# Optimization experiments

Hardware: AMD Instinct MI355X
Metric: run time of the kernel (lower is better)

## Reference

```python
import jax, jax.numpy as jnp
import numpy as np

D_MODEL = 1024
N_HEADS = 16
HEAD_DIM = D_MODEL // N_HEADS


def setup_inputs() -> dict:
    key = jax.random.key(0)
    ks = jax.random.split(key, 9)
    s = 1.0 / np.sqrt(D_MODEL)
    inp = {
        "x": jax.random.normal(ks[0], (4, 2048, D_MODEL), dtype=jnp.float32),
        "wq": jax.random.uniform(ks[1], (D_MODEL, D_MODEL), jnp.float32, -s, s),
        "bq": jax.random.uniform(ks[2], (D_MODEL,), jnp.float32, -s, s),
        "wk": jax.random.uniform(ks[3], (D_MODEL, D_MODEL), jnp.float32, -s, s),
        "bk": jax.random.uniform(ks[4], (D_MODEL,), jnp.float32, -s, s),
        "wv": jax.random.uniform(ks[5], (D_MODEL, D_MODEL), jnp.float32, -s, s),
        "bv": jax.random.uniform(ks[6], (D_MODEL,), jnp.float32, -s, s),
        "wo": jax.random.uniform(ks[7], (D_MODEL, D_MODEL), jnp.float32, -s, s),
        "bo": jax.random.uniform(ks[8], (D_MODEL,), jnp.float32, -s, s),
    }
    return inp


def reference(x, wq, bq, wk, bk, wv, bv, wo, bo):
    b, s, d = x.shape
    h, hd = N_HEADS, HEAD_DIM
    # projections (torch Linear: y = x @ W.T + b; here weights stored as [in, out])
    q = (x @ wq + bq).reshape(b, s, h, hd).transpose(0, 2, 1, 3)  # [b,h,s,hd]
    k = (x @ wk + bk).reshape(b, s, h, hd).transpose(0, 2, 1, 3)
    v = (x @ wv + bv).reshape(b, s, h, hd).transpose(0, 2, 1, 3)
    scores = jnp.einsum("bhqd,bhkd->bhqk", q, k) / jnp.sqrt(jnp.float32(hd))
    causal = jnp.tril(jnp.ones((s, s), dtype=bool))
    scores = jnp.where(causal, scores, -jnp.inf)
    weights = jax.nn.softmax(scores, axis=-1)
    attn = jnp.einsum("bhqk,bhkd->bhqd", weights, v)  # [b,h,s,hd]
    attn = attn.transpose(0, 2, 1, 3).reshape(b, s, d)
    return attn @ wo + bo
```

## Files before the change

### kernel.cpp

```cpp
#include <hip/hip_runtime.h>
#include <cstddef>

#define D_MODEL 1024
#define NH 16
#define HD 64
#define BATCH 4
#define SEQ 2048
#define MTOT (BATCH * SEQ)

typedef _Float16 half8 __attribute__((ext_vector_type(8)));
typedef _Float16 half4v __attribute__((ext_vector_type(4)));
typedef float f32x4 __attribute__((ext_vector_type(4)));

#if __has_builtin(__builtin_amdgcn_exp2f)
#define EXP2(x) __builtin_amdgcn_exp2f(x)
#else
#define EXP2(x) __expf((x)*0.69314718056f)
#endif

__global__ __launch_bounds__(256) void prep(
    const float* __restrict__ x, _Float16* __restrict__ xh,
    const float* __restrict__ W0, const float* __restrict__ W1,
    const float* __restrict__ W2, const float* __restrict__ W3,
    _Float16* __restrict__ T0, _Float16* __restrict__ T1,
    _Float16* __restrict__ T2, _Float16* __restrict__ T3)
{
    __shared__ float T[64][65];
    const int bid = blockIdx.x;
    if (bid < 256) {
        const size_t base = (size_t)bid * 4096 + threadIdx.x;
#pragma unroll
        for (int it = 0; it < 16; ++it) {
            const size_t i = base + (size_t)it * 256;
            const float4* p = (const float4*)x + 2 * i;
            float4 a = p[0], b = p[1];
            half8 h;
            h[0] = (_Float16)a.x; h[1] = (_Float16)a.y; h[2] = (_Float16)a.z; h[3] = (_Float16)a.w;
            h[4] = (_Float16)b.x; h[5] = (_Float16)b.y; h[6] = (_Float16)b.z; h[7] = (_Float16)b.w;
            *((half8*)xh + i) = h;
        }
    } else {
        const int t = bid - 256;
        const int mtx = t >> 8;
        const float* W = (mtx == 0) ? W0 : (mtx == 1) ? W1 : (mtx == 2) ? W2 : W3;
        _Float16*   Wt = (mtx == 0) ? T0 : (mtx == 1) ? T1 : (mtx == 2) ? T2 : T3;
        const int tile = t & 255;
        const int k0 = (tile >> 4) * 64, n0 = (tile & 15) * 64;
        const int r = threadIdx.x >> 4, c4 = (threadIdx.x & 15) * 4;

#pragma unroll
        for (int i = 0; i < 4; ++i) {
            float4 v = *(const float4*)(W + (size_t)(k0 + r + 16 * i) * 1024 + n0 + c4);
            T[r + 16 * i][c4 + 0] = v.x; T[r + 16 * i][c4 + 1] = v.y;
            T[r + 16 * i][c4 + 2] = v.z; T[r + 16 * i][c4 + 3] = v.w;
        }
        __syncthreads();
#pragma unroll
        for (int i = 0; i < 4; ++i) {
            const int n = r + 16 * i;
            half4v h;
            h[0] = (_Float16)T[c4 + 0][n]; h[1] = (_Float16)T[c4 + 1][n];
            h[2] = (_Float16)T[c4 + 2][n]; h[3] = (_Float16)T[c4 + 3][n];
            *(half4v*)(Wt + (size_t)(n0 + n) * 1024 + k0 + c4) = h;
        }
    }
}

template <int QKV>
__global__ __launch_bounds__(256) void gemm_mfma(
    const _Float16* __restrict__ A,
    const _Float16* __restrict__ Bt0, const _Float16* __restrict__ Bt1, const _Float16* __restrict__ Bt2,
    const float* __restrict__ bi0, const float* __restrict__ bi1, const float* __restrict__ bi2,
    void* __restrict__ C0, void* __restrict__ C1, void* __restrict__ C2)
{
    const int L = blockIdx.x;
    const int y = L & 63;
    const int c_ = L >> 6;
    const int z  = QKV ? (c_ >> 3) : 0;
    const int xb = QKV ? (c_ & 7) : c_;

    const _Float16* Bt = (z == 0) ? Bt0 : (z == 1) ? Bt1 : Bt2;
    const float*   bia = (z == 0) ? bi0 : (z == 1) ? bi1 : bi2;
    void*            C = (z == 0) ? C0  : (z == 1) ? C1  : C2;

    __shared__ _Float16 As[128][72];
    __shared__ _Float16 Bs[128][72];

    const int tid  = threadIdx.x;
    const int w    = tid >> 6;
    const int lane = tid & 63;
    const int l15  = lane & 15;
    const int lg   = lane >> 4;
    const int m0 = y * 128;
    const int n0 = xb * 128;
    const int wm = (w >> 1) * 64, wn = (w & 1) * 64;

    const int srow = tid >> 3;
    const int scol = (tid & 7) * 8;

    const _Float16* Ab = A + (size_t)(m0 + srow) * 1024 + scol;
    const _Float16* Bb = Bt + (size_t)(n0 + srow) * 1024 + scol;

    half8 aR[4], bR[4];
#pragma unroll
    for (int i = 0; i < 4; ++i) {
        aR[i] = *(const half8*)(Ab + (size_t)(32 * i) * 1024);
        bR[i] = *(const half8*)(Bb + (size_t)(32 * i) * 1024);
    }

    f32x4 acc[4][4];
#pragma unroll
    for (int i = 0; i < 4; ++i)
#pragma unroll
        for (int j = 0; j < 4; ++j) { acc[i][j][0] = 0.f; acc[i][j][1] = 0.f; acc[i][j][2] = 0.f; acc[i][j][3] = 0.f; }

    for (int kt = 0; kt < 16; ++kt) {
        __syncthreads();
#pragma unroll
        for (int i = 0; i < 4; ++i) {
            *(half8*)&As[srow + 32 * i][scol] = aR[i];
            *(half8*)&Bs[srow + 32 * i][scol] = bR[i];
        }
        __syncthreads();
        if (kt < 15) {
            const int k0 = (kt + 1) * 64;
#pragma unroll
            for (int i = 0; i < 4; ++i) {
                aR[i] = *(const half8*)(Ab + (size_t)(32 * i) * 1024 + k0);
                bR[i] = *(const half8*)(Bb + (size_t)(32 * i) * 1024 + k0);
            }
        }
#pragma unroll
        for (int c = 0; c < 2; ++c) {
            half8 af[4], bf[4];
#pragma unroll
            for (int i = 0; i < 4; ++i) af[i] = *(const half8*)&As[wm + 16 * i + l15][32 * c + 8 * lg];
#pragma unroll
            for (int j = 0; j < 4; ++j) bf[j] = *(const half8*)&Bs[wn + 16 * j + l15][32 * c + 8 * lg];
#pragma unroll
            for (int i = 0; i < 4; ++i)
#pragma unroll
                for (int j = 0; j < 4; ++j)
                    acc[i][j] = __builtin_amdgcn_mfma_f32_16x16x32_f16(af[i], bf[j], acc[i][j], 0, 0, 0);
        }
    }

    float bv[4];
#pragma unroll
    for (int j = 0; j < 4; ++j) bv[j] = bia[n0 + wn + 16 * j + l15];

#pragma unroll
    for (int i = 0; i < 4; ++i)
#pragma unroll
        for (int j = 0; j < 4; ++j)
#pragma unroll
            for (int r = 0; r < 4; ++r) {
                const int m = m0 + wm + 16 * i + 4 * lg + r;
                const int n = n0 + wn + 16 * j + l15;
                const float val = acc[i][j][r] + bv[j];
                if (QKV) {
                    const int bb = m >> 11, ss = m & 2047, hh = n >> 6, hd = n & 63;
                    if (z < 2)
                        ((_Float16*)C)[((size_t)(bb * NH + hh) * SEQ + ss) * HD + hd] = (_Float16)val;
                    else
                        ((_Float16*)C)[((size_t)(bb * NH + hh) * HD + hd) * SEQ + ss] = (_Float16)val;
                } else {
                    ((float*)C)[(size_t)m * 1024 + n] = val;
                }
            }
}

__global__ __launch_bounds__(256, 4) void attn_fwd_mfma(
    const _Float16* __restrict__ Q, const _Float16* __restrict__ K,
    const _Float16* __restrict__ Vt, _Float16* __restrict__ O)
{
    __shared__ _Float16 Ks[64][80];
    __shared__ _Float16 Vs[64][80];
    __shared__ _Float16 Ps[4][16][80];

    const int tid  = threadIdx.x;
    const int w    = tid >> 6;
    const int lane = tid & 63;
    const int l15  = lane & 15;
    const int lg   = lane >> 4;

    const int bh = blockIdx.y;
    const int b  = bh >> 4, h = bh & 15;

    const _Float16* Qb  = Q  + (size_t)bh * SEQ * HD;
    const _Float16* Kb  = K  + (size_t)bh * SEQ * HD;
    const _Float16* Vtb = Vt + (size_t)bh * HD * SEQ;

    const int srow = tid >> 3;
    const int scol = (tid & 7) * 8;

    for (int pass = 0; pass < 2; ++pass) {
        const int qt = pass ? (int)blockIdx.x : (31 - (int)blockIdx.x);
        const int q0 = qt * 64;
        const int ntiles = qt + 1;

        half8 qa[2];
        {
            const _Float16* qp = Qb + (size_t)(q0 + 16 * w + l15) * HD + 8 * lg;
            qa[0] = *(const half8*)(qp);
            qa[1] = *(const half8*)(qp + 32);
#pragma unroll
            for (int c = 0; c < 2; ++c)
#pragma unroll
                for (int j = 0; j < 8; ++j)
                    qa[c][j] = (_Float16)((float)qa[c][j] * 0.18033688f);
        }

        f32x4 o_[4];
#pragma unroll
        for (int ft = 0; ft < 4; ++ft) { o_[ft][0] = 0.f; o_[ft][1] = 0.f; o_[ft][2] = 0.f; o_[ft][3] = 0.f; }
        float lp[4] = {0.f, 0.f, 0.f, 0.f};

        half8 kreg[2], vreg[2];
#pragma unroll
        for (int j = 0; j < 2; ++j) {
            kreg[j] = *(const half8*)(Kb  + (size_t)(srow + 32 * j) * HD + scol);
            vreg[j] = *(const half8*)(Vtb + (size_t)(srow + 32 * j) * SEQ + scol);
        }

        for (int kt = 0; kt < ntiles; ++kt) {
            __syncthreads();
#pragma unroll
            for (int j = 0; j < 2; ++j) {
                *(half8*)&Ks[srow + 32 * j][scol] = kreg[j];
                *(half8*)&Vs[srow + 32 * j][scol] = vreg[j];
            }
            __syncthreads();

            if (kt + 1 < ntiles) {
                const int k0 = (kt + 1) * 64;
#pragma unroll
                for (int j = 0; j < 2; ++j) {
                    kreg[j] = *(const half8*)(Kb  + (size_t)(k0 + srow + 32 * j) * HD + scol);
                    vreg[j] = *(const half8*)(Vtb + (size_t)(srow + 32 * j) * SEQ + k0 + scol);
                }
            }

            f32x4 s[4];
#pragma unroll
            for (int f = 0; f < 4; ++f) { s[f][0] = 0.f; s[f][1] = 0.f; s[f][2] = 0.f; s[f][3] = 0.f; }
#pragma unroll
            for (int c = 0; c < 2; ++c)
#pragma unroll
                for (int f = 0; f < 4; ++f) {
                    half8 kb = *(const half8*)&Ks[16 * f + l15][32 * c + 8 * lg];
                    s[f] = __builtin_amdgcn_mfma_f32_16x16x32_f16(qa[c], kb, s[f], 0, 0, 0);
                }

            const bool dg = (kt == qt);
#pragma unroll
            for (int f = 0; f < 4; ++f)
#pragma unroll
                for (int r = 0; r < 4; ++r) {
                    float p = EXP2(s[f][r]);
                    if (dg && (16 * f + l15 > 16 * w + 4 * lg + r)) p = 0.f;
                    lp[r] += p;
                    Ps[w][4 * lg + r][16 * f + l15] = (_Float16)p;
                }

            half8 pa[2];
            pa[0] = *(const half8*)&Ps[w][l15][8 * lg];
            pa[1] = *(const half8*)&Ps[w][l15][32 + 8 * lg];
#pragma unroll
            for (int c = 0; c < 2; ++c)
#pragma unroll
                for (int ft = 0; ft < 4; ++ft) {
                    half8 vb = *(const half8*)&Vs[16 * ft + l15][32 * c + 8 * lg];
                    o_[ft] = __builtin_amdgcn_mfma_f32_16x16x32_f16(pa[c], vb, o_[ft], 0, 0, 0);
                }
        }

#pragma unroll
        for (int r = 0; r < 4; ++r) {
            float rs = lp[r];
            rs += __shfl_xor(rs, 1);
            rs += __shfl_xor(rs, 2);
            rs += __shfl_xor(rs, 4);
            rs += __shfl_xor(rs, 8);
            const float inv = 1.0f / rs;
            _Float16* orow = O + (size_t)(b * SEQ + q0 + 16 * w + 4 * lg + r) * D_MODEL + h * HD + l15;
#pragma unroll
            for (int ft = 0; ft < 4; ++ft) orow[16 * ft] = (_Float16)(o_[ft][r] * inv);
        }
        __syncthreads();
    }
}

extern "C" void kernel_launch(void* const* d_in, const int* in_sizes, int n_in,
                              void* d_out, int out_size, void* d_ws, size_t ws_size,
                              hipStream_t stream)
{
    const float* x  = (const float*)d_in[0];
    const float* wq = (const float*)d_in[1];
    const float* bq = (const float*)d_in[2];
    const float* wk = (const float*)d_in[3];
    const float* bk = (const float*)d_in[4];
    const float* wv = (const float*)d_in[5];
    const float* bv = (const float*)d_in[6];
    const float* wo = (const float*)d_in[7];
    const float* bo = (const float*)d_in[8];
    float* out = (float*)d_out;

    const size_t SZ = (size_t)MTOT * D_MODEL;
    const size_t WZ = (size_t)D_MODEL * D_MODEL;

    _Float16* xh  = (_Float16*)d_ws;
    _Float16* wtq = xh + SZ;
    _Float16* wtk = wtq + WZ;
    _Float16* wtv = wtk + WZ;
    _Float16* wto = wtv + WZ;
    _Float16* Qh  = wto + WZ;
    _Float16* Kh  = Qh + SZ;
    _Float16* Vtg = Kh + SZ;
    _Float16* AOh = Vtg + SZ;

    prep<<<dim3(1280), 256, 0, stream>>>(x, xh, wq, wk, wv, wo, wtq, wtk, wtv, wto);
    gemm_mfma<1><<<dim3(1536), 256, 0, stream>>>(xh, wtq, wtk, wtv, bq, bk, bv, Qh, Kh, Vtg);
    attn_fwd_mfma<<<dim3(16, BATCH * NH), 256, 0, stream>>>(Qh, Kh, Vtg, AOh);
    gemm_mfma<0><<<dim3(512), 256, 0, stream>>>(AOh, wto, wto, wto, bo, bo, bo, out, out, out);
}
```

Baseline: 271.2 us.

## Load GEMM tiles directly into LDS with XOR-swizzled layout

The projection GEMM now copies A and B tiles from global memory straight into shared memory using async global-to-LDS loads. This replaces the register-staged prefetch. The shared tiles drop their padding and use an XOR swizzle on 16-byte chunks to avoid bank conflicts. This saves registers and LDS write instructions, but the next tile is no longer prefetched during compute, so load latency is exposed each iteration.

```diff
diff --git a/kernel.cpp b/kernel.cpp
--- a/kernel.cpp
+++ b/kernel.cpp
@@ -17,6 +17,15 @@
 #else
 #define EXP2(x) __expf((x)*0.69314718056f)
 #endif
+
+#define ASYNC_COPY16(g, l)                                                    \
+    __builtin_amdgcn_global_load_lds(                                         \
+        (__attribute__((address_space(1))) const void*)(g),                   \
+        (__attribute__((address_space(3))) void*)(l), 16, 0, 0)
+
+#define LDSFRAG(S, R, CH)                                                     \
+    (*(const half8*)((const char*)(S) + ((R) << 7) +                          \
+                     ((((CH) << 1)) ^ (((R) & 7) << 4))))
 
 __global__ __launch_bounds__(256) void prep(
     const float* __restrict__ x, _Float16* __restrict__ xh,
@@ -83,8 +92,8 @@
     const float*   bia = (z == 0) ? bi0 : (z == 1) ? bi1 : bi2;
     void*            C = (z == 0) ? C0  : (z == 1) ? C1  : C2;
 
-    __shared__ _Float16 As[128][72];
-    __shared__ _Float16 Bs[128][72];
+    __shared__ _Float16 As[128][64];
+    __shared__ _Float16 Bs[128][64];
 
     const int tid  = threadIdx.x;
     const int w    = tid >> 6;
@@ -95,18 +104,13 @@
     const int n0 = xb * 128;
     const int wm = (w >> 1) * 64, wn = (w & 1) * 64;
 
-    const int srow = tid >> 3;
-    const int scol = (tid & 7) * 8;
-
-    const _Float16* Ab = A + (size_t)(m0 + srow) * 1024 + scol;
-    const _Float16* Bb = Bt + (size_t)(n0 + srow) * 1024 + scol;
-
-    half8 aR[4], bR[4];
-#pragma unroll
-    for (int i = 0; i < 4; ++i) {
-        aR[i] = *(const half8*)(Ab + (size_t)(32 * i) * 1024);
-        bR[i] = *(const half8*)(Bb + (size_t)(32 * i) * 1024);
-    }
+    const int rsub = lane >> 3;
+    const int cswz = ((lane & 7) ^ rsub) * 8;
+
+    const _Float16* gA = A  + (size_t)(m0 + 32 * w + rsub) * 1024 + cswz;
+    const _Float16* gB = Bt + (size_t)(n0 + 32 * w + rsub) * 1024 + cswz;
+    char* lA = (char*)As + (size_t)(w * 4) * 1024;
+    char* lB = (char*)Bs + (size_t)(w * 4) * 1024;
 
     f32x4 acc[4][4];
 #pragma unroll
@@ -115,28 +119,22 @@
         for (int j = 0; j < 4; ++j) { acc[i][j][0] = 0.f; acc[i][j][1] = 0.f; acc[i][j][2] = 0.f; acc[i][j][3] = 0.f; }
 
     for (int kt = 0; kt < 16; ++kt) {
+        const int k0 = kt * 64;
         __syncthreads();
 #pragma unroll
         for (int i = 0; i < 4; ++i) {
-            *(half8*)&As[srow + 32 * i][scol] = aR[i];
-            *(half8*)&Bs[srow + 32 * i][scol] = bR[i];
+            ASYNC_COPY16(gA + (size_t)(8 * i) * 1024 + k0, lA + i * 1024);
+            ASYNC_COPY16(gB + (size_t)(8 * i) * 1024 + k0, lB + i * 1024);
         }
         __syncthreads();
-        if (kt < 15) {
-            const int k0 = (kt + 1) * 64;
-#pragma unroll
-            for (int i = 0; i < 4; ++i) {
-                aR[i] = *(const half8*)(Ab + (size_t)(32 * i) * 1024 + k0);
-                bR[i] = *(const half8*)(Bb + (size_t)(32 * i) * 1024 + k0);
-            }
-        }
+
 #pragma unroll
         for (int c = 0; c < 2; ++c) {
             half8 af[4], bf[4];
 #pragma unroll
-            for (int i = 0; i < 4; ++i) af[i] = *(const half8*)&As[wm + 16 * i + l15][32 * c + 8 * lg];
-#pragma unroll
-            for (int j = 0; j < 4; ++j) bf[j] = *(const half8*)&Bs[wn + 16 * j + l15][32 * c + 8 * lg];
+            for (int i = 0; i < 4; ++i) af[i] = LDSFRAG(As, wm + 16 * i + l15, 32 * c + 8 * lg);
+#pragma unroll
+            for (int j = 0; j < 4; ++j) bf[j] = LDSFRAG(Bs, wn + 16 * j + l15, 32 * c + 8 * lg);
 #pragma unroll
             for (int i = 0; i < 4; ++i)
 #pragma unroll
@@ -145,9 +143,9 @@
         }
     }
 
-    float bv[4];
-#pragma unroll
-    for (int j = 0; j < 4; ++j) bv[j] = bia[n0 + wn + 16 * j + l15];
+    float bvv[4];
+#pragma unroll
+    for (int j = 0; j < 4; ++j) bvv[j] = bia[n0 + wn + 16 * j + l15];
 
 #pragma unroll
     for (int i = 0; i < 4; ++i)
@@ -157,7 +155,7 @@
             for (int r = 0; r < 4; ++r) {
                 const int m = m0 + wm + 16 * i + 4 * lg + r;
                 const int n = n0 + wn + 16 * j + l15;
-                const float val = acc[i][j][r] + bv[j];
+                const float val = acc[i][j][r] + bvv[j];
                 if (QKV) {
                     const int bb = m >> 11, ss = m & 2047, hh = n >> 6, hd = n & 63;
                     if (z < 2)
```

New measurement: 269.3 us. Within noise of the previous version (-0.7%).
